# Kernel optimization log

Measured on AMD Instinct MI355X. Metric: run time of the kernel, lower is better.

Reference implementation:

```python
import jax, jax.numpy as jnp
import numpy as np
from jax import lax

B, T, D_IN, D_H, D_OUT = 64, 512, 256, 1024, 256


def setup_inputs() -> dict:
    key = jax.random.key(0)
    k1, k2, k3, k4 = jax.random.split(key, 4)
    # lecun_normal-style scaling: std = 1/sqrt(fan_in)
    inputs = jax.random.normal(k1, (B, T, D_IN), dtype=jnp.float32)
    input_kernel = jax.random.normal(k2, (D_IN, D_H), dtype=jnp.float32) / np.sqrt(D_IN)
    hidden_kernel = jax.random.normal(k3, (D_H, D_H), dtype=jnp.float32) / np.sqrt(D_H)
    hidden_bias = jnp.zeros((D_H,), dtype=jnp.float32)
    output_kernel = jax.random.normal(k4, (D_H, D_OUT), dtype=jnp.float32) / np.sqrt(D_H)
    output_bias = jnp.zeros((D_OUT,), dtype=jnp.float32)
    return {
        "inputs": inputs,
        "input_kernel": input_kernel,
        "hidden_kernel": hidden_kernel,
        "hidden_bias": hidden_bias,
        "output_kernel": output_kernel,
        "output_bias": output_bias,
    }


def reference(inputs, input_kernel, hidden_kernel, hidden_bias, output_kernel, output_bias):
    # inputs: [B, T, D_in]. Precompute the input projection for all timesteps
    # (batched GEMM) — same math as per-step x_t @ W_in inside scan.
    x_proj = jnp.einsum("bti,ih->bth", inputs, input_kernel) + hidden_bias  # [B,T,H]
    x_proj_tm = jnp.swapaxes(x_proj, 0, 1)  # time-major [T,B,H]

    def step(h, xp_t):
        h_new = jnp.tanh(xp_t + jnp.dot(h, hidden_kernel))  # [B,H]
        return h_new, h_new

    h0 = jnp.zeros((inputs.shape[0], hidden_kernel.shape[0]), dtype=inputs.dtype)
    _, hidden_states = lax.scan(step, h0, x_proj_tm)  # [T,B,H]
    hidden_states = jnp.swapaxes(hidden_states, 0, 1)  # [B,T,H]
    # Dense readout applied to every timestep (return_sequences=True)
    outputs = jnp.einsum("bth,ho->bto", hidden_states, output_kernel) + output_bias
    return outputs
```

## Files before the change

### kernel.cpp

```cpp
#include <hip/hip_runtime.h>
#include <stdint.h>
#include <stddef.h>


#define TT 512
#define HH 1024

typedef __attribute__((ext_vector_type(8))) short short8;
typedef __attribute__((ext_vector_type(4))) float f32x4;
typedef unsigned long long u64;

#define POISON 0xAAAAAAAAAAAAAAAAull

__device__ inline short f2bf(float f) {
  uint32_t u = __builtin_bit_cast(uint32_t, f);
  u += 0x7fffu + ((u >> 16) & 1u);
  return (short)(u >> 16);
}

__device__ inline float fast_tanh(float x) {
  float ax = fabsf(x);
  float e = __expf(-2.f * ax);
  float r = (1.f - e) * __builtin_amdgcn_rcpf(1.f + e);
  return copysignf(r, x);
}

__global__ __launch_bounds__(256, 1) void xproj_kernel(
    const float* __restrict__ inp,
    const float* __restrict__ w_in,
    const float* __restrict__ h_b,
    float* __restrict__ xp) {
  const int blk = blockIdx.x;
  const int c = blk & 3, s = blk >> 2;
  const int tid = threadIdx.x;
  const int wv = tid >> 6, l = tid & 63, lr = l & 15, lq = l >> 4;

  __shared__ short ldsA[16 * 264];

  short8 wf[8][4];
#pragma unroll
  for (int kt = 0; kt < 8; ++kt)
#pragma unroll
    for (int nt = 0; nt < 4; ++nt) {
      int col = c * 256 + (wv * 4 + nt) * 16 + lr;
      int k0 = kt * 32 + lq * 8;
      short8 v;
#pragma unroll
      for (int e = 0; e < 8; ++e) v[e] = f2bf(w_in[(size_t)(k0 + e) * HH + col]);
      wf[kt][nt] = v;
    }
  float bias[4];
#pragma unroll
  for (int nt = 0; nt < 4; ++nt) bias[nt] = h_b[c * 256 + (wv * 4 + nt) * 16 + lr];

  for (int it = 0; it < 8; ++it) {
    int m = s + 256 * it;
    int t = m >> 2, g = m & 3;
    {
      int row = tid >> 4, cb = (tid & 15) * 16;
      const float* src = inp + ((size_t)(g * 16 + row) * TT + t) * 256 + cb;
      f32x4 v0 = *(const f32x4*)(src);
      f32x4 v1 = *(const f32x4*)(src + 4);
      f32x4 v2 = *(const f32x4*)(src + 8);
      f32x4 v3 = *(const f32x4*)(src + 12);
      short8 sa, sb;
      sa[0]=f2bf(v0[0]); sa[1]=f2bf(v0[1]); sa[2]=f2bf(v0[2]); sa[3]=f2bf(v0[3]);
      sa[4]=f2bf(v1[0]); sa[5]=f2bf(v1[1]); sa[6]=f2bf(v1[2]); sa[7]=f2bf(v1[3]);
      sb[0]=f2bf(v2[0]); sb[1]=f2bf(v2[1]); sb[2]=f2bf(v2[2]); sb[3]=f2bf(v2[3]);
      sb[4]=f2bf(v3[0]); sb[5]=f2bf(v3[1]); sb[6]=f2bf(v3[2]); sb[7]=f2bf(v3[3]);
      *(short8*)&ldsA[row * 264 + cb] = sa;
      *(short8*)&ldsA[row * 264 + cb + 8] = sb;
    }
    __syncthreads();

    f32x4 acc[4];
#pragma unroll
    for (int nt = 0; nt < 4; ++nt) acc[nt] = (f32x4){0.f, 0.f, 0.f, 0.f};
#pragma unroll
    for (int kt = 0; kt < 8; ++kt) {
      short8 a = *(const short8*)&ldsA[lr * 264 + kt * 32 + lq * 8];
#pragma unroll
      for (int nt = 0; nt < 4; ++nt)
        acc[nt] = __builtin_amdgcn_mfma_f32_16x16x32_bf16(a, wf[kt][nt], acc[nt], 0, 0, 0);
    }
#pragma unroll
    for (int nt = 0; nt < 4; ++nt) {
      f32x4 o;
#pragma unroll
      for (int i2 = 0; i2 < 4; ++i2) o[i2] = acc[nt][i2] + bias[nt];
      *(f32x4*)(xp + ((size_t)(t * 4 + g) * 64 + c * 16 + wv * 4 + nt) * 256 + l * 4) = o;
    }
    __syncthreads();
  }
}

__global__ __launch_bounds__(256, 1) void scan_kernel(
    const float* __restrict__ xp, const float* __restrict__ w_h,
    short* __restrict__ hbuf) {
  const int blk = blockIdx.x;
  const int g = blk & 3, j = blk >> 2;
  const int tid = threadIdx.x;
  const int wv = tid >> 6, l = tid & 63, lr = l & 15, lq = l >> 4;
  const int ntg = j * 4 + wv;

  __shared__ f32x4 red[2][4][4][64];
  __shared__ short ldsw[4][16 * 24];

  short8 wf[8][4];
#pragma unroll
  for (int f = 0; f < 8; ++f)
#pragma unroll
    for (int nt = 0; nt < 4; ++nt) {
      int n = j * 64 + nt * 16 + lr;
      int k0 = wv * 256 + f * 32 + lq * 8;
      short8 v;
#pragma unroll
      for (int e = 0; e < 8; ++e) v[e] = f2bf(w_h[(size_t)(k0 + e) * HH + n]);
      wf[f][nt] = v;
    }

  const u64* hq = (const u64*)hbuf;
  u64* hqw = (u64*)hbuf;

  for (int t = 0; t < TT; ++t) {
    f32x4 xpv = *(const f32x4*)(xp + ((size_t)(t * 4 + g) * 64 + ntg) * 256 + l * 4);

    f32x4 acc[4];
#pragma unroll
    for (int nt = 0; nt < 4; ++nt) acc[nt] = (f32x4){0.f, 0.f, 0.f, 0.f};

    if (t > 0) {
      u64 q[16];
      size_t base = (((size_t)((t - 1) * 4 + g) * 32 + wv * 8) * 64 + l) * 2;
      int bad;
      do {
#pragma unroll
        for (int f = 0; f < 8; ++f) {
          q[2 * f]     = __hip_atomic_load(hq + base + (size_t)f * 128,
                                           __ATOMIC_RELAXED, __HIP_MEMORY_SCOPE_AGENT);
          q[2 * f + 1] = __hip_atomic_load(hq + base + (size_t)f * 128 + 1,
                                           __ATOMIC_RELAXED, __HIP_MEMORY_SCOPE_AGENT);
        }
        int mybad = 0;
#pragma unroll
        for (int i = 0; i < 16; ++i) mybad |= (q[i] == POISON);
        bad = __any(mybad);
      } while (bad);

      short8 af[8];
#pragma unroll
      for (int f = 0; f < 8; ++f) {
        union { u64 qq[2]; short8 s; } u;
        u.qq[0] = q[2 * f];
        u.qq[1] = q[2 * f + 1];
        af[f] = u.s;
      }
#pragma unroll
      for (int f = 0; f < 8; ++f)
#pragma unroll
        for (int nt = 0; nt < 4; ++nt)
          acc[nt] = __builtin_amdgcn_mfma_f32_16x16x32_bf16(af[f], wf[f][nt], acc[nt], 0, 0, 0);
    }

    const int bi = t & 1;
    f32x4 own = acc[0];
#pragma unroll
    for (int nt = 0; nt < 4; ++nt) {
      if (nt == wv) own = acc[nt];
      else red[bi][wv][nt][l] = acc[nt];
    }
    __syncthreads();

    f32x4 tot = own;
#pragma unroll
    for (int p = 0; p < 4; ++p)
      if (p != wv) tot += red[bi][p][wv][l];

    short* lw = &ldsw[wv][0];
#pragma unroll
    for (int i2 = 0; i2 < 4; ++i2) {
      float v = tot[i2] + xpv[i2];
      lw[(lq * 4 + i2) * 24 + lr] = f2bf(fast_tanh(v));
    }
    if (l < 32) {
      short8 hv = *(const short8*)&lw[(l & 15) * 24 + (l >> 4) * 8];
      union { short8 s; u64 qq[2]; } u;
      u.s = hv;
      const int kt = 2 * j + (wv >> 1);
      size_t wb = ((size_t)(t * 4 + g) * 32 + kt) * 128 +
                  ((size_t)(l + 32 * (wv & 1))) * 2;
      (void)__hip_atomic_exchange(hqw + wb, u.qq[0],
                                  __ATOMIC_RELAXED, __HIP_MEMORY_SCOPE_AGENT);
      (void)__hip_atomic_exchange(hqw + wb + 1, u.qq[1],
                                  __ATOMIC_RELAXED, __HIP_MEMORY_SCOPE_AGENT);
    }
  }
}

__global__ __launch_bounds__(256, 1) void outproj_kernel(
    const short* __restrict__ hbuf, const float* __restrict__ w_o,
    const float* __restrict__ o_b, float* __restrict__ out) {
  const int blk = blockIdx.x;
  const int c = blk & 3, s = blk >> 2;
  const int tid = threadIdx.x;
  const int wv = tid >> 6, l = tid & 63, lr = l & 15, lq = l >> 4;

  __shared__ f32x4 red[4][4][64];

  short8 wf[8][4];
#pragma unroll
  for (int f = 0; f < 8; ++f)
#pragma unroll
    for (int nt = 0; nt < 4; ++nt) {
      int o = c * 64 + nt * 16 + lr;
      int k0 = wv * 256 + f * 32 + lq * 8;
      short8 v;
#pragma unroll
      for (int e = 0; e < 8; ++e) v[e] = f2bf(w_o[(size_t)(k0 + e) * 256 + o]);
      wf[f][nt] = v;
    }
  float bias = o_b[c * 64 + wv * 16 + lr];
  const short8* hfr = (const short8*)hbuf;

  for (int it = 0; it < 8; ++it) {
    int m = s + 256 * it;
    int t = m >> 2, g = m & 3;
    short8 af[8];
    size_t base = ((size_t)(t * 4 + g) * 32 + wv * 8) * 64 + l;
#pragma unroll
    for (int f = 0; f < 8; ++f) af[f] = hfr[base + (size_t)f * 64];
    f32x4 acc[4];
#pragma unroll
    for (int nt = 0; nt < 4; ++nt) acc[nt] = (f32x4){0.f, 0.f, 0.f, 0.f};
#pragma unroll
    for (int f = 0; f < 8; ++f)
#pragma unroll
      for (int nt = 0; nt < 4; ++nt)
        acc[nt] = __builtin_amdgcn_mfma_f32_16x16x32_bf16(af[f], wf[f][nt], acc[nt], 0, 0, 0);

    red[wv][0][l] = acc[0];
    red[wv][1][l] = acc[1];
    red[wv][2][l] = acc[2];
    red[wv][3][l] = acc[3];
    __syncthreads();
    f32x4 tot = red[0][wv][l] + red[1][wv][l] + red[2][wv][l] + red[3][wv][l];
#pragma unroll
    for (int i2 = 0; i2 < 4; ++i2) {
      int b = g * 16 + lq * 4 + i2;
      out[((size_t)b * TT + t) * 256 + c * 64 + wv * 16 + lr] = tot[i2] + bias;
    }
    __syncthreads();
  }
}

extern "C" void kernel_launch(void* const* d_in, const int* in_sizes, int n_in,
                              void* d_out, int out_size, void* d_ws, size_t ws_size,
                              hipStream_t stream) {
  const float* inp  = (const float*)d_in[0];
  const float* w_in = (const float*)d_in[1];
  const float* w_h  = (const float*)d_in[2];
  const float* h_b  = (const float*)d_in[3];
  const float* w_o  = (const float*)d_in[4];
  const float* o_b  = (const float*)d_in[5];

  float* xp   = (float*)d_ws;
  short* hbuf = (short*)((char*)d_ws + (size_t)134217728);

  xproj_kernel<<<1024, 256, 0, stream>>>(inp, w_in, h_b, xp);
  scan_kernel<<<64, 256, 0, stream>>>(xp, w_h, hbuf);
  outproj_kernel<<<1024, 256, 0, stream>>>(hbuf, w_o, o_b, (float*)d_out);
}
```

Before: 1.454 ms.

## Store input projection as bf16 and add per-step sentinel flags to scan

```diff
diff --git a/kernel.cpp b/kernel.cpp
--- a/kernel.cpp
+++ b/kernel.cpp
@@ -7,6 +7,7 @@
 #define HH 1024
 
 typedef __attribute__((ext_vector_type(8))) short short8;
+typedef __attribute__((ext_vector_type(4))) short s16x4;
 typedef __attribute__((ext_vector_type(4))) float f32x4;
 typedef unsigned long long u64;
 
@@ -16,6 +17,11 @@
   uint32_t u = __builtin_bit_cast(uint32_t, f);
   u += 0x7fffu + ((u >> 16) & 1u);
   return (short)(u >> 16);
+}
+
+__device__ inline float bf2f(short s) {
+  uint32_t u = ((uint32_t)(uint16_t)s) << 16;
+  return __builtin_bit_cast(float, u);
 }
 
 __device__ inline float fast_tanh(float x) {
@@ -29,7 +35,7 @@
     const float* __restrict__ inp,
     const float* __restrict__ w_in,
     const float* __restrict__ h_b,
-    float* __restrict__ xp) {
+    short* __restrict__ xp) {
   const int blk = blockIdx.x;
   const int c = blk & 3, s = blk >> 2;
   const int tid = threadIdx.x;
@@ -85,25 +91,25 @@
     }
 #pragma unroll
     for (int nt = 0; nt < 4; ++nt) {
-      f32x4 o;
-#pragma unroll
-      for (int i2 = 0; i2 < 4; ++i2) o[i2] = acc[nt][i2] + bias[nt];
-      *(f32x4*)(xp + ((size_t)(t * 4 + g) * 64 + c * 16 + wv * 4 + nt) * 256 + l * 4) = o;
+      s16x4 o;
+#pragma unroll
+      for (int i2 = 0; i2 < 4; ++i2) o[i2] = f2bf(acc[nt][i2] + bias[nt]);
+      *(s16x4*)(xp + ((size_t)(t * 4 + g) * 64 + c * 16 + wv * 4 + nt) * 256 + l * 4) = o;
     }
     __syncthreads();
   }
 }
 
 __global__ __launch_bounds__(256, 1) void scan_kernel(
-    const float* __restrict__ xp, const float* __restrict__ w_h,
-    short* __restrict__ hbuf) {
+    const short* __restrict__ xp, const float* __restrict__ w_h,
+    short* __restrict__ hbuf, int* __restrict__ sent) {
   const int blk = blockIdx.x;
   const int g = blk & 3, j = blk >> 2;
   const int tid = threadIdx.x;
   const int wv = tid >> 6, l = tid & 63, lr = l & 15, lq = l >> 4;
   const int ntg = j * 4 + wv;
 
-  __shared__ f32x4 red[2][4][4][64];
+  __shared__ f32x4 red[4][4][64];
   __shared__ short ldsw[4][16 * 24];
 
   short8 wf[8][4];
@@ -123,7 +129,16 @@
   u64* hqw = (u64*)hbuf;
 
   for (int t = 0; t < TT; ++t) {
-    f32x4 xpv = *(const f32x4*)(xp + ((size_t)(t * 4 + g) * 64 + ntg) * 256 + l * 4);
+    s16x4 xps = *(const s16x4*)(xp + ((size_t)(t * 4 + g) * 64 + ntg) * 256 + l * 4);
+
+    if (t > 0 && wv == 0) {
+      const int* sp = sent + ((size_t)(t - 1) * 4 + g) * 64;
+      int v;
+      do {
+        v = __hip_atomic_load(sp + l, __ATOMIC_RELAXED, __HIP_MEMORY_SCOPE_AGENT);
+      } while (__any(v != t - 1));
+    }
+    __syncthreads();
 
     f32x4 acc[4];
 #pragma unroll
@@ -162,38 +177,40 @@
           acc[nt] = __builtin_amdgcn_mfma_f32_16x16x32_bf16(af[f], wf[f][nt], acc[nt], 0, 0, 0);
     }
 
-    const int bi = t & 1;
     f32x4 own = acc[0];
 #pragma unroll
     for (int nt = 0; nt < 4; ++nt) {
       if (nt == wv) own = acc[nt];
-      else red[bi][wv][nt][l] = acc[nt];
+      else red[wv][nt][l] = acc[nt];
     }
     __syncthreads();
 
     f32x4 tot = own;
 #pragma unroll
     for (int p = 0; p < 4; ++p)
-      if (p != wv) tot += red[bi][p][wv][l];
+      if (p != wv) tot += red[p][wv][l];
 
     short* lw = &ldsw[wv][0];
 #pragma unroll
     for (int i2 = 0; i2 < 4; ++i2) {
-      float v = tot[i2] + xpv[i2];
+      float v = tot[i2] + bf2f(xps[i2]);
       lw[(lq * 4 + i2) * 24 + lr] = f2bf(fast_tanh(v));
     }
+    const int kt = 2 * j + (wv >> 1);
     if (l < 32) {
       short8 hv = *(const short8*)&lw[(l & 15) * 24 + (l >> 4) * 8];
       union { short8 s; u64 qq[2]; } u;
       u.s = hv;
-      const int kt = 2 * j + (wv >> 1);
       size_t wb = ((size_t)(t * 4 + g) * 32 + kt) * 128 +
                   ((size_t)(l + 32 * (wv & 1))) * 2;
-      (void)__hip_atomic_exchange(hqw + wb, u.qq[0],
-                                  __ATOMIC_RELAXED, __HIP_MEMORY_SCOPE_AGENT);
-      (void)__hip_atomic_exchange(hqw + wb + 1, u.qq[1],
-                                  __ATOMIC_RELAXED, __HIP_MEMORY_SCOPE_AGENT);
-    }
+      __hip_atomic_store(hqw + wb, u.qq[0],
+                         __ATOMIC_RELAXED, __HIP_MEMORY_SCOPE_AGENT);
+      __hip_atomic_store(hqw + wb + 1, u.qq[1],
+                         __ATOMIC_RELAXED, __HIP_MEMORY_SCOPE_AGENT);
+    }
+    if (l == 0)
+      __hip_atomic_store(sent + ((size_t)t * 4 + g) * 64 + kt * 2 + (wv & 1), t,
+                         __ATOMIC_RELAXED, __HIP_MEMORY_SCOPE_AGENT);
   }
 }
 
@@ -263,10 +280,11 @@
   const float* w_o  = (const float*)d_in[4];
   const float* o_b  = (const float*)d_in[5];
 
-  float* xp   = (float*)d_ws;
-  short* hbuf = (short*)((char*)d_ws + (size_t)134217728);
+  short* xp   = (short*)d_ws;
+  short* hbuf = (short*)((char*)d_ws + (size_t)67108864);
+  int*   sent = (int*)((char*)d_ws + (size_t)134217728);
 
   xproj_kernel<<<1024, 256, 0, stream>>>(inp, w_in, h_b, xp);
-  scan_kernel<<<64, 256, 0, stream>>>(xp, w_h, hbuf);
+  scan_kernel<<<64, 256, 0, stream>>>(xp, w_h, hbuf, sent);
   outproj_kernel<<<1024, 256, 0, stream>>>(hbuf, w_o, o_b, (float*)d_out);
 }
```

New measurement: 1.709 ms. 1.18x slower.
